# Performance work log

Hardware: AMD Instinct MI355X
Metric: run time of the kernel (lower is better)

The kernel has to match this reference:

```python
import math
import jax, jax.numpy as jnp
import numpy as np


def _sph_harm_abs(colat, L):
    """|Y_l^m| for l=1..L, m=-l..l, evaluated with polar argument = colat.
    Matches |scipy.special.sph_harm(m, l, theta, phi=colat)| since |exp(i m theta)|=1.
    colat: [N,T,V,V]. Returns [N, L^2+2L, T, V, V].
    """
    ct = jnp.cos(colat)
    s = jnp.abs(jnp.sin(colat))  # (1-ct^2)^{1/2}
    # Associated Legendre P_l^m(ct) (Condon-Shortley phase irrelevant under abs)
    P = {(0, 0): jnp.ones_like(ct)}
    for m in range(1, L + 1):
        P[(m, m)] = (2 * m - 1) * s * P[(m - 1, m - 1)]
    for m in range(0, L):
        P[(m + 1, m)] = (2 * m + 1) * ct * P[(m, m)]
    for m in range(0, L + 1):
        for l in range(m + 2, L + 1):
            P[(l, m)] = ((2 * l - 1) * ct * P[(l - 1, m)] - (l + m - 1) * P[(l - 2, m)]) / (l - m)
    terms = []
    for l in range(1, L + 1):
        for m in range(-l, l + 1):
            am = abs(m)
            norm = math.sqrt((2 * l + 1) / (4.0 * math.pi)
                             * math.factorial(l - am) / math.factorial(l + am))
            terms.append(jnp.float32(norm) * jnp.abs(P[(l, am)]))
    return jnp.stack(terms, axis=1)  # [N, Lm, T, V, V]


def setup_inputs() -> dict:
    key = jax.random.key(0)
    x = jax.random.normal(key, (32, 3, 256, 25), dtype=jnp.float32)
    return {"x": x, "l_range": 3}


def reference(x, l_range):
    N, C, T, V = x.shape
    # local_coord: pairwise joint differences -> [N,3,T,V,V]
    d = x[:, :, :, :, None] - x[:, :, :, None, :]
    # Spherical_coord: the module passes colatitude=atan2(y,x) as scipy's polar arg
    colat = jnp.arctan2(d[:, 1], d[:, 0])  # [N,T,V,V]
    # |Y_l^m|: the exp(i m theta) phase vanishes under abs()
    y = _sph_harm_abs(colat, int(l_range))  # [N, Lm, T, V, V]
    Lm = y.shape[1]
    # permute(0,1,4,2,3).view(N, Lm*V, T, V)
    out = jnp.transpose(y, (0, 1, 4, 2, 3)).reshape(N, Lm * V, T, V)
    return out.astype(jnp.float32)
```

## Files before the change

### kernel.cpp

```cpp
#include <hip/hip_runtime.h>
#include <math.h>

#define NV   25
#define NT   256
#define LMCH 15
#define LMSTRIDE (NV * NT * NV)
#define PLANE (NT * NV)
#define NGRP (PLANE / 4)
#define NPLANES (32 * NV)
#define NGRP_TOTAL (NPLANES * NGRP)
#define GRID 2048
#define STRIDE (GRID * 256)

__global__ __launch_bounds__(256)
void sym_kernel(const float* __restrict__ x, float* __restrict__ out) {
    const int cmap[15] = {0, 1, 0, 2, 3, 4, 3, 2, 5, 6, 7, 8, 7, 6, 5};

    for (int G = blockIdx.x * 256 + threadIdx.x; G < NGRP_TOTAL; G += STRIDE) {
        const int plane = G / NGRP;
        const int gg    = G - plane * NGRP;
        const int p0    = gg * 4;
        const int n     = plane / NV;
        const int j     = plane - n * NV;

        const float* __restrict__ xb0 = x + n * 3 * PLANE;
        const float* __restrict__ xb1 = xb0 + PLANE;
        float* __restrict__ ob = out + n * (LMCH * PLANE * NV) + j * PLANE;

        const float4 xi0 = *reinterpret_cast<const float4*>(xb0 + p0);
        const float4 xi1 = *reinterpret_cast<const float4*>(xb1 + p0);
        const float xi0a[4] = {xi0.x, xi0.y, xi0.z, xi0.w};
        const float xi1a[4] = {xi1.x, xi1.y, xi1.z, xi1.w};

        float yd[9][4];

        #pragma unroll
        for (int k = 0; k < 4; ++k) {
            const int p = p0 + k;
            const int t = p / NV;
            const float xj0 = xb0[t * NV + j];
            const float xj1 = xb1[t * NV + j];

            const float dx = xi0a[k] - xj0;
            const float dy = xi1a[k] - xj1;
            const float r2 = dx * dx + dy * dy;

            const float rinv = (r2 > 0.0f) ? rsqrtf(r2) : 0.0f;
            const float ct   = (r2 > 0.0f) ? dx * rinv : 1.0f;
            const float s    = fabsf(dy) * rinv;

            const float act = fabsf(ct);
            const float c2  = ct * ct;
            const float s2  = s * s;

            yd[0][k] = 0.34549415f * s;
            yd[1][k] = 0.48860252f * act;
            yd[2][k] = 0.38627420f * s2;
            yd[3][k] = 0.77254841f * act * s;
            yd[4][k] = 0.31539157f * fabsf(3.0f * c2 - 1.0f);
            yd[5][k] = 0.41722381f * s2 * s;
            yd[6][k] = 1.02198547f * act * s2;
            yd[7][k] = 0.32318002f * fabsf(5.0f * c2 - 1.0f) * s;
            yd[8][k] = act * fabsf(1.86588166f * c2 - 1.11952898f);
        }

        #pragma unroll
        for (int c = 0; c < 15; ++c) {
            const int d = cmap[c];
            *reinterpret_cast<float4*>(ob + c * LMSTRIDE + p0) =
                make_float4(yd[d][0], yd[d][1], yd[d][2], yd[d][3]);
        }
    }
}

extern "C" void kernel_launch(void* const* d_in, const int* in_sizes, int n_in,
                              void* d_out, int out_size, void* d_ws, size_t ws_size,
                              hipStream_t stream) {
    const float* x = (const float*)d_in[0];
    float* out = (float*)d_out;
    sym_kernel<<<GRID, 256, 0, stream>>>(x, out);
}
```

Measured before the change: 52.81 us.

## Map each thread to one output float4 for fully contiguous stores

Switches the parallel decomposition from one thread per input group writing 15 strided channel outputs to one thread per output float4, indexed linearly so stores are perfectly contiguous across the grid. Each thread recomputes the angular quantities and selects the single harmonic needed for its channel through a switch on lm. This aims to improve write coalescing and locality of the output stream, at the cost of recomputing the geometry up to 15 times and re-reading inputs per channel.

```diff
diff --git a/kernel.cpp b/kernel.cpp
--- a/kernel.cpp
+++ b/kernel.cpp
@@ -1,38 +1,36 @@
 #include <hip/hip_runtime.h>
 #include <math.h>
 
-#define NV   25
-#define NT   256
-#define LMCH 15
-#define LMSTRIDE (NV * NT * NV)
-#define PLANE (NT * NV)
-#define NGRP (PLANE / 4)
-#define NPLANES (32 * NV)
-#define NGRP_TOTAL (NPLANES * NGRP)
-#define GRID 2048
+#define NV     25
+#define NT     256
+#define PLANE  (NT * NV)
+#define NCH    (15 * NV)
+#define GPP    (PLANE / 4)
+#define GPN    (NCH * GPP)
+#define NG_OUT (32 * GPN)
+#define GRID   2048
 #define STRIDE (GRID * 256)
 
 __global__ __launch_bounds__(256)
 void sym_kernel(const float* __restrict__ x, float* __restrict__ out) {
-    const int cmap[15] = {0, 1, 0, 2, 3, 4, 3, 2, 5, 6, 7, 8, 7, 6, 5};
-
-    for (int G = blockIdx.x * 256 + threadIdx.x; G < NGRP_TOTAL; G += STRIDE) {
-        const int plane = G / NGRP;
-        const int gg    = G - plane * NGRP;
-        const int p0    = gg * 4;
-        const int n     = plane / NV;
-        const int j     = plane - n * NV;
+    for (int G = blockIdx.x * 256 + threadIdx.x; G < NG_OUT; G += STRIDE) {
+        const int n   = G / GPN;
+        const int r1  = G - n * GPN;
+        const int ch  = r1 / GPP;
+        const int g   = r1 - ch * GPP;
+        const int p0  = g * 4;
+        const int lm  = ch / NV;
+        const int j   = ch - lm * NV;
 
         const float* __restrict__ xb0 = x + n * 3 * PLANE;
         const float* __restrict__ xb1 = xb0 + PLANE;
-        float* __restrict__ ob = out + n * (LMCH * PLANE * NV) + j * PLANE;
 
         const float4 xi0 = *reinterpret_cast<const float4*>(xb0 + p0);
         const float4 xi1 = *reinterpret_cast<const float4*>(xb1 + p0);
         const float xi0a[4] = {xi0.x, xi0.y, xi0.z, xi0.w};
         const float xi1a[4] = {xi1.x, xi1.y, xi1.z, xi1.w};
 
-        float yd[9][4];
+        float sA[4], actA[4], c2A[4], s2A[4];
 
         #pragma unroll
         for (int k = 0; k < 4; ++k) {
@@ -49,27 +47,32 @@
             const float ct   = (r2 > 0.0f) ? dx * rinv : 1.0f;
             const float s    = fabsf(dy) * rinv;
 
-            const float act = fabsf(ct);
-            const float c2  = ct * ct;
-            const float s2  = s * s;
-
-            yd[0][k] = 0.34549415f * s;
-            yd[1][k] = 0.48860252f * act;
-            yd[2][k] = 0.38627420f * s2;
-            yd[3][k] = 0.77254841f * act * s;
-            yd[4][k] = 0.31539157f * fabsf(3.0f * c2 - 1.0f);
-            yd[5][k] = 0.41722381f * s2 * s;
-            yd[6][k] = 1.02198547f * act * s2;
-            yd[7][k] = 0.32318002f * fabsf(5.0f * c2 - 1.0f) * s;
-            yd[8][k] = act * fabsf(1.86588166f * c2 - 1.11952898f);
+            sA[k]   = s;
+            actA[k] = fabsf(ct);
+            c2A[k]  = ct * ct;
+            s2A[k]  = s * s;
         }
 
+        float v[4];
         #pragma unroll
-        for (int c = 0; c < 15; ++c) {
-            const int d = cmap[c];
-            *reinterpret_cast<float4*>(ob + c * LMSTRIDE + p0) =
-                make_float4(yd[d][0], yd[d][1], yd[d][2], yd[d][3]);
+        for (int k = 0; k < 4; ++k) {
+            const float s = sA[k], act = actA[k], c2 = c2A[k], s2 = s2A[k];
+            float y;
+            switch (lm) {
+            case 0: case 2:  y = 0.34549415f * s; break;
+            case 1:          y = 0.48860252f * act; break;
+            case 3: case 7:  y = 0.38627420f * s2; break;
+            case 4: case 6:  y = 0.77254841f * act * s; break;
+            case 5:          y = 0.31539157f * fabsf(3.0f * c2 - 1.0f); break;
+            case 8: case 14: y = 0.41722381f * s2 * s; break;
+            case 9: case 13: y = 1.02198547f * act * s2; break;
+            case 10: case 12: y = 0.32318002f * fabsf(5.0f * c2 - 1.0f) * s; break;
+            default:         y = act * fabsf(1.86588166f * c2 - 1.11952898f); break;
+            }
+            v[k] = y;
         }
+
+        reinterpret_cast<float4*>(out)[G] = make_float4(v[0], v[1], v[2], v[3]);
     }
 }
 
```

New measurement: 132.7 us. 151% more time.
